# Kernel optimization log

Hardware: AMD Instinct MI355X
Metric: run time of the kernel (lower is better)

## Reference

```python
import jax, jax.numpy as jnp
import numpy as np

N, E = 50000, 800000
IN_DIM, HEADS, OUT_DIM = 128, 4, 32
NEG_SLOPE = 0.2
EPS = 1e-16


def setup_inputs() -> dict:
    key = jax.random.key(0)
    k = jax.random.split(key, 6)
    x = jax.random.normal(k[0], (N, IN_DIM), dtype=jnp.float32)
    edge_index = jax.random.randint(k[1], (2, E), 0, N, dtype=jnp.int64)
    # xavier-uniform-ish params
    lim_w = float(np.sqrt(6.0 / (IN_DIM + HEADS * OUT_DIM)))
    W = jax.random.uniform(k[2], (HEADS * OUT_DIM, IN_DIM), minval=-lim_w, maxval=lim_w, dtype=jnp.float32)
    lim_a = float(np.sqrt(6.0 / (1 + HEADS * OUT_DIM)))
    att_src = jax.random.uniform(k[3], (1, HEADS, OUT_DIM), minval=-lim_a, maxval=lim_a, dtype=jnp.float32)
    att_dst = jax.random.uniform(k[4], (1, HEADS, OUT_DIM), minval=-lim_a, maxval=lim_a, dtype=jnp.float32)
    bias = jnp.zeros((HEADS * OUT_DIM,), dtype=jnp.float32)
    return {"x": x, "edge_index": edge_index, "W": W, "att_src": att_src, "att_dst": att_dst, "bias": bias}


def reference(x, edge_index, W, att_src, att_dst, bias):
    n = x.shape[0]
    h = (x @ W.T).reshape(n, HEADS, OUT_DIM)           # (N,H,D)
    src, dst = edge_index[0], edge_index[1]
    a_src = jnp.sum(h * att_src, axis=-1)              # (N,H)
    a_dst = jnp.sum(h * att_dst, axis=-1)              # (N,H)
    alpha = a_src[src] + a_dst[dst]                    # (E,H)
    alpha = jax.nn.leaky_relu(alpha, NEG_SLOPE)
    # segment (per-dst) softmax over edges, per head
    m = jax.ops.segment_max(alpha, dst, num_segments=n)   # (N,H)
    ex = jnp.exp(alpha - m[dst])
    s = jax.ops.segment_sum(ex, dst, num_segments=n)      # (N,H)
    alpha = ex / (s[dst] + EPS)                            # (E,H)
    # dropout p=0 (eval) -> identity
    msg = h[src] * alpha[..., None]                        # (E,H,D)
    out = jax.ops.segment_sum(msg, dst, num_segments=n)    # (N,H,D)
    out = out.reshape(n, HEADS * OUT_DIM) + bias
    alpha_pooled = alpha.mean(axis=-1)                     # (E,)
    return out, alpha_pooled
```

## Files before the change

### kernel.cpp

```cpp
#include <hip/hip_runtime.h>

#define NNODES 50000
#define NEDGES 800000
#define HD 128
#define NEG 0.2f
#define MTILE 64
#define LDW 136
#define MAXD 64
#define GEMMB ((NNODES + MTILE - 1) / MTILE)
#define NBINS 196
#define CAP 5120
#define GST 16
#define ABLK ((NEDGES + 2047) / 2048)

typedef __attribute__((ext_vector_type(8))) short short8;
typedef __attribute__((ext_vector_type(4))) float floatx4;

static __device__ inline unsigned short f2bf(float f) {
    unsigned u = __float_as_uint(f);
    return (unsigned short)((u + 0x7FFF + ((u >> 16) & 1)) >> 16);
}
static __device__ inline float bf2f(unsigned short u) {
    return __uint_as_float(((unsigned)u) << 16);
}
static __device__ inline float lrelu_exp(float a) {
    a = (a > 0.f) ? a : NEG * a;
    return __expf(a);
}

__global__ __launch_bounds__(256, 4) void gat_main(
    const float* __restrict__ x, const float* __restrict__ W,
    const float* __restrict__ att_src, const float* __restrict__ att_dst,
    const int* __restrict__ ei,
    unsigned short* __restrict__ h, float* __restrict__ asrc,
    float* __restrict__ adst, int* __restrict__ gcnt, int* __restrict__ cbuf)
{
    __shared__ unsigned short Wl[128 * LDW];
    const int t = threadIdx.x;

    if (blockIdx.x >= GEMMB) {
        int* hist = (int*)Wl;
        int* boff = hist + 256;
        const int e0 = (blockIdx.x - GEMMB) * 2048 + t * 8;
        const bool act = (e0 < NEDGES);
        int4 s0 = make_int4(0, 0, 0, 0), s1 = s0, d0 = s0, d1 = s0;
        if (act) {
            s0 = *(const int4*)(ei + e0);
            s1 = *(const int4*)(ei + e0 + 4);
            d0 = *(const int4*)(ei + NEDGES + e0);
            d1 = *(const int4*)(ei + NEDGES + e0 + 4);
        }
        hist[t] = 0;
        __syncthreads();
        if (act) {
            atomicAdd(&hist[d0.x >> 8], 1); atomicAdd(&hist[d0.y >> 8], 1);
            atomicAdd(&hist[d0.z >> 8], 1); atomicAdd(&hist[d0.w >> 8], 1);
            atomicAdd(&hist[d1.x >> 8], 1); atomicAdd(&hist[d1.y >> 8], 1);
            atomicAdd(&hist[d1.z >> 8], 1); atomicAdd(&hist[d1.w >> 8], 1);
        }
        __syncthreads();
        if (t < NBINS && hist[t] > 0)
            boff[t] = atomicAdd(&gcnt[t * GST], hist[t]);
        __syncthreads();
        if (act) {
            int ss[8] = {s0.x, s0.y, s0.z, s0.w, s1.x, s1.y, s1.z, s1.w};
            int dd[8] = {d0.x, d0.y, d0.z, d0.w, d1.x, d1.y, d1.z, d1.w};
#pragma unroll
            for (int j = 0; j < 8; j++) {
                int b = dd[j] >> 8;
                int slot = atomicAdd(&boff[b], 1);
                cbuf[(size_t)b * CAP + slot] = ((dd[j] & 255) << 16) | ss[j];
            }
        }
        return;
    }

    const int rowBase = blockIdx.x * MTILE;

    for (int idx = t * 8; idx < 128 * 128; idx += 2048) {
        int r = idx >> 7, c = idx & 127;
        float4 v0 = *(const float4*)(W + idx);
        float4 v1 = *(const float4*)(W + idx + 4);
        short8 u;
        u[0] = (short)f2bf(v0.x); u[1] = (short)f2bf(v0.y);
        u[2] = (short)f2bf(v0.z); u[3] = (short)f2bf(v0.w);
        u[4] = (short)f2bf(v1.x); u[5] = (short)f2bf(v1.y);
        u[6] = (short)f2bf(v1.z); u[7] = (short)f2bf(v1.w);
        *(short8*)(Wl + r * LDW + c) = u;
    }

    const int wave = t >> 6;
    const int lane = t & 63;
    const int c16  = lane & 15;
    const int quad = lane >> 4;
    const int xr   = rowBase + wave * 16 + c16;
    short8 av[4];
#pragma unroll
    for (int kc = 0; kc < 4; kc++) {
        float4 v0 = make_float4(0.f, 0.f, 0.f, 0.f);
        float4 v1 = v0;
        if (xr < NNODES) {
            const float* p = x + (size_t)xr * 128 + kc * 32 + quad * 8;
            v0 = *(const float4*)p;
            v1 = *(const float4*)(p + 4);
        }
        short8 u;
        u[0] = (short)f2bf(v0.x); u[1] = (short)f2bf(v0.y);
        u[2] = (short)f2bf(v0.z); u[3] = (short)f2bf(v0.w);
        u[4] = (short)f2bf(v1.x); u[5] = (short)f2bf(v1.y);
        u[6] = (short)f2bf(v1.z); u[7] = (short)f2bf(v1.w);
        av[kc] = u;
    }
    __syncthreads();

    floatx4 acc[8];
#pragma unroll
    for (int nt = 0; nt < 8; nt++) acc[nt] = (floatx4)(0.f);

#pragma unroll
    for (int kc = 0; kc < 4; kc++) {
#pragma unroll
        for (int nt = 0; nt < 8; nt++) {
            short8 bv = *(const short8*)(Wl + (nt * 16 + c16) * LDW + kc * 32 + quad * 8);
            acc[nt] = __builtin_amdgcn_mfma_f32_16x16x32_bf16(av[kc], bv, acc[nt], 0, 0, 0);
        }
    }

    float As[8], Ad[8];
#pragma unroll
    for (int nt = 0; nt < 8; nt++) {
        As[nt] = att_src[nt * 16 + c16];
        Ad[nt] = att_dst[nt * 16 + c16];
    }
#pragma unroll
    for (int r = 0; r < 4; r++) {
        const int gr = rowBase + wave * 16 + quad * 4 + r;
#pragma unroll
        for (int hh = 0; hh < 4; hh++) {
            float ps = acc[2 * hh][r] * As[2 * hh] + acc[2 * hh + 1][r] * As[2 * hh + 1];
            float pd = acc[2 * hh][r] * Ad[2 * hh] + acc[2 * hh + 1][r] * Ad[2 * hh + 1];
#pragma unroll
            for (int m = 8; m >= 1; m >>= 1) {
                ps += __shfl_xor(ps, m, 64);
                pd += __shfl_xor(pd, m, 64);
            }
            if (c16 == 0 && gr < NNODES) {
                asrc[gr * 4 + hh] = ps;
                adst[gr * 4 + hh] = pd;
            }
        }
    }

    __syncthreads();
#pragma unroll
    for (int r = 0; r < 4; r++) {
        const int lr = wave * 16 + quad * 4 + r;
#pragma unroll
        for (int nt = 0; nt < 8; nt++)
            Wl[lr * LDW + nt * 16 + c16] = f2bf(acc[nt][r]);
    }
    __syncthreads();
    for (int idx = t * 8; idx < MTILE * 128; idx += 2048) {
        int r = idx >> 7, c = idx & 127;
        int g = rowBase + r;
        if (g < NNODES)
            *(short8*)(h + (size_t)g * HD + c) = *(const short8*)(Wl + r * LDW + c);
    }
}

__global__ __launch_bounds__(1024) void gat_bin(
    const int* __restrict__ gcnt, const int* __restrict__ cbuf,
    int* __restrict__ coff, unsigned short* __restrict__ csr)
{
    __shared__ unsigned short eb[CAP];
    __shared__ int sh[256], hist[256], run[256];
    const int t = threadIdx.x;
    const int b = blockIdx.x;
    const int c_b = gcnt[b * GST];
    const size_t wbase = (size_t)b * CAP;

    if (t < 256) {
        sh[t] = (t < NBINS) ? gcnt[t * GST] : 0;
        hist[t] = 0;
    }
    __syncthreads();
    for (int off = 1; off < 256; off <<= 1) {
        int u = (t < 256 && t >= off) ? sh[t - off] : 0;
        __syncthreads();
        if (t < 256) sh[t] += u;
        __syncthreads();
    }
    const int binbase = sh[b] - c_b;

    for (int i = t; i < c_b; i += 1024)
        atomicAdd(&hist[(cbuf[wbase + i] >> 16) & 255], 1);
    __syncthreads();

    int hv = 0;
    if (t < 256) { hv = hist[t]; sh[t] = hv; }
    __syncthreads();
    for (int off = 1; off < 256; off <<= 1) {
        int u = (t < 256 && t >= off) ? sh[t - off] : 0;
        __syncthreads();
        if (t < 256) sh[t] += u;
        __syncthreads();
    }
    if (t < 256) {
        int ex = sh[t] - hv;
        int n = b * 256 + t;
        if (n < NNODES) coff[n] = binbase + ex;
        run[t] = ex;
    }
    if (b == 0 && t == 0) coff[NNODES] = NEDGES;
    __syncthreads();

    for (int i = t; i < c_b; i += 1024) {
        int e = cbuf[wbase + i];
        int slot = atomicAdd(&run[(e >> 16) & 255], 1);
        eb[slot] = (unsigned short)(e & 0xFFFF);
    }
    __syncthreads();

    for (int i = t; i < c_b; i += 1024)
        csr[binbase + i] = eb[i];
}

__global__ __launch_bounds__(256) void gat_node(
    const int* __restrict__ coff, const unsigned short* __restrict__ csr,
    const float* __restrict__ asrc, const float* __restrict__ adst,
    const unsigned short* __restrict__ h, const float* __restrict__ bias,
    float* __restrict__ out, float* __restrict__ rsumr)
{
    __shared__ unsigned short sh_src[8 * MAXD];
    __shared__ float sh_w[8 * MAXD * 4];
    const int t = threadIdx.x;
    const int node8 = t >> 5;
    const int n = blockIdx.x * 8 + node8;
    const int k = t & 31;
    const int beg = coff[n], end = coff[n + 1];
    const int base = node8 * MAXD;
    const float4 bn = *(const float4*)(adst + n * 4);

    float4 sum = make_float4(0.f, 0.f, 0.f, 0.f);
    for (int j = beg + k; j < end; j += 32) {
        int s = csr[j];
        float4 a = *(const float4*)(asrc + s * 4);
        float4 wv;
        wv.x = lrelu_exp(a.x + bn.x);
        wv.y = lrelu_exp(a.y + bn.y);
        wv.z = lrelu_exp(a.z + bn.z);
        wv.w = lrelu_exp(a.w + bn.w);
        sum.x += wv.x; sum.y += wv.y; sum.z += wv.z; sum.w += wv.w;
        int i = j - beg;
        if (i < MAXD) {
            sh_src[base + i] = (unsigned short)s;
            *(float4*)(sh_w + (base + i) * 4) = wv;
        }
    }
#pragma unroll
    for (int m = 16; m >= 1; m >>= 1) {
        sum.x += __shfl_xor(sum.x, m, 64);
        sum.y += __shfl_xor(sum.y, m, 64);
        sum.z += __shfl_xor(sum.z, m, 64);
        sum.w += __shfl_xor(sum.w, m, 64);
    }
    float rs[4];
    rs[0] = 1.f / (sum.x + 1e-16f);
    rs[1] = 1.f / (sum.y + 1e-16f);
    rs[2] = 1.f / (sum.z + 1e-16f);
    rs[3] = 1.f / (sum.w + 1e-16f);
    if (k == 0)
        *(float4*)(rsumr + n * 4) = make_float4(rs[0], rs[1], rs[2], rs[3]);

    const int half = k >> 4;
    const int i16  = k & 15;
    const int head = i16 >> 2;
    const float rsel = rs[head];
    const int lim = (end - beg < MAXD) ? end - beg : MAXD;

    float accA[8], accB[8];
#pragma unroll
    for (int m = 0; m < 8; m++) { accA[m] = 0.f; accB[m] = 0.f; }

    int j = 0;
    for (; j + 8 <= lim; j += 8) {
        int e0 = j + half, e1 = j + 2 + half, e2 = j + 4 + half, e3 = j + 6 + half;
        int s0 = sh_src[base + e0];
        int s1 = sh_src[base + e1];
        int s2 = sh_src[base + e2];
        int s3 = sh_src[base + e3];
        float w0 = sh_w[(base + e0) * 4 + head] * rsel;
        float w1 = sh_w[(base + e1) * 4 + head] * rsel;
        float w2 = sh_w[(base + e2) * 4 + head] * rsel;
        float w3 = sh_w[(base + e3) * 4 + head] * rsel;
        short8 u0 = *(const short8*)(h + (size_t)s0 * HD + i16 * 8);
        short8 u1 = *(const short8*)(h + (size_t)s1 * HD + i16 * 8);
        short8 u2 = *(const short8*)(h + (size_t)s2 * HD + i16 * 8);
        short8 u3 = *(const short8*)(h + (size_t)s3 * HD + i16 * 8);
#pragma unroll
        for (int m = 0; m < 8; m++) {
            accA[m] = fmaf(bf2f((unsigned short)u0[m]), w0, accA[m]);
            accB[m] = fmaf(bf2f((unsigned short)u1[m]), w1, accB[m]);
            accA[m] = fmaf(bf2f((unsigned short)u2[m]), w2, accA[m]);
            accB[m] = fmaf(bf2f((unsigned short)u3[m]), w3, accB[m]);
        }
    }
    for (; j + 2 <= lim; j += 2) {
        int e0 = j + half;
        int s0 = sh_src[base + e0];
        float w0 = sh_w[(base + e0) * 4 + head] * rsel;
        short8 u0 = *(const short8*)(h + (size_t)s0 * HD + i16 * 8);
#pragma unroll
        for (int m = 0; m < 8; m++)
            accA[m] = fmaf(bf2f((unsigned short)u0[m]), w0, accA[m]);
    }
    if (j < lim && half == 0) {
        int s0 = sh_src[base + j];
        float w0 = sh_w[(base + j) * 4 + head] * rsel;
        short8 u0 = *(const short8*)(h + (size_t)s0 * HD + i16 * 8);
#pragma unroll
        for (int m = 0; m < 8; m++)
            accA[m] = fmaf(bf2f((unsigned short)u0[m]), w0, accA[m]);
    }
    const float bnh = ((const float*)&bn)[head];
    for (int jj = beg + MAXD + half; jj < end; jj += 2) {
        int s0 = csr[jj];
        float w0 = lrelu_exp(asrc[s0 * 4 + head] + bnh) * rsel;
        short8 u0 = *(const short8*)(h + (size_t)s0 * HD + i16 * 8);
#pragma unroll
        for (int m = 0; m < 8; m++)
            accA[m] = fmaf(bf2f((unsigned short)u0[m]), w0, accA[m]);
    }

#pragma unroll
    for (int m = 0; m < 8; m++) {
        accA[m] += accB[m];
        accA[m] += __shfl_xor(accA[m], 16, 64);
    }
    const float4 b4 = *(const float4*)(bias + i16 * 8 + half * 4);
    float4 st;
    st.x = accA[half * 4 + 0] + b4.x;
    st.y = accA[half * 4 + 1] + b4.y;
    st.z = accA[half * 4 + 2] + b4.z;
    st.w = accA[half * 4 + 3] + b4.w;
    *(float4*)(out + (size_t)n * HD + i16 * 8 + half * 4) = st;
}

static __device__ inline float apool1(
    int s, int d, const float* __restrict__ asrc,
    const float* __restrict__ adst, const float* __restrict__ rsumr)
{
    float4 a = *(const float4*)(asrc + s * 4);
    float4 b = *(const float4*)(adst + d * 4);
    float4 r = *(const float4*)(rsumr + d * 4);
    return 0.25f * (lrelu_exp(a.x + b.x) * r.x + lrelu_exp(a.y + b.y) * r.y +
                    lrelu_exp(a.z + b.z) * r.z + lrelu_exp(a.w + b.w) * r.w);
}

__global__ __launch_bounds__(256) void gat_apool(
    const int* __restrict__ ei, const float* __restrict__ asrc,
    const float* __restrict__ adst, const float* __restrict__ rsumr,
    float* __restrict__ apool)
{
    int e0 = (blockIdx.x * 256 + threadIdx.x) * 4;
    if (e0 >= NEDGES) return;
    int4 s = *(const int4*)(ei + e0);
    int4 d = *(const int4*)(ei + NEDGES + e0);
    float4 r;
    r.x = apool1(s.x, d.x, asrc, adst, rsumr);
    r.y = apool1(s.y, d.y, asrc, adst, rsumr);
    r.z = apool1(s.z, d.z, asrc, adst, rsumr);
    r.w = apool1(s.w, d.w, asrc, adst, rsumr);
    *(float4*)(apool + e0) = r;
}

extern "C" void kernel_launch(void* const* d_in, const int* in_sizes, int n_in,
                              void* d_out, int out_size, void* d_ws, size_t ws_size,
                              hipStream_t stream)
{
    const float* x       = (const float*)d_in[0];
    const int*   ei      = (const int*)d_in[1];
    const float* W       = (const float*)d_in[2];
    const float* att_src = (const float*)d_in[3];
    const float* att_dst = (const float*)d_in[4];
    const float* bias    = (const float*)d_in[5];

    float* out   = (float*)d_out;
    float* apool = out + (size_t)NNODES * HD;

    unsigned short* h = (unsigned short*)d_ws;
    float* asrc  = (float*)(h + (size_t)NNODES * HD);
    float* adst  = asrc + NNODES * 4;
    float* rsumr = adst + NNODES * 4;
    int*   gcnt  = (int*)(rsumr + NNODES * 4);
    int*   coff  = gcnt + NBINS * GST;
    int*   cbuf  = coff + NNODES + 4;
    unsigned short* csr = (unsigned short*)(cbuf + (size_t)NBINS * CAP);

    hipMemsetAsync(gcnt, 0, (size_t)NBINS * GST * sizeof(int), stream);

    gat_main<<<GEMMB + ABLK, 256, 0, stream>>>(
        x, W, att_src, att_dst, ei, h, asrc, adst, gcnt, cbuf);
    gat_bin<<<NBINS, 1024, 0, stream>>>(gcnt, cbuf, coff, csr);
    gat_node<<<NNODES / 8, 256, 0, stream>>>(
        coff, csr, asrc, adst, h, bias, out, rsumr);
    gat_apool<<<(NEDGES / 4 + 255) / 256, 256, 0, stream>>>(
        ei, asrc, adst, rsumr, apool);
}
```

Before: 167.7 us.

## Replace global atomic binning with per-block local sort and one wave per node

```diff
diff --git a/kernel.cpp b/kernel.cpp
--- a/kernel.cpp
+++ b/kernel.cpp
@@ -10,7 +10,6 @@
 #define GEMMB ((NNODES + MTILE - 1) / MTILE)
 #define NBINS 196
 #define CAP 5120
-#define GST 16
 #define ABLK ((NEDGES + 2047) / 2048)
 
 typedef __attribute__((ext_vector_type(8))) short short8;
@@ -33,16 +32,20 @@
     const float* __restrict__ att_src, const float* __restrict__ att_dst,
     const int* __restrict__ ei,
     unsigned short* __restrict__ h, float* __restrict__ asrc,
-    float* __restrict__ adst, int* __restrict__ gcnt, int* __restrict__ cbuf)
-{
-    __shared__ unsigned short Wl[128 * LDW];
+    float* __restrict__ adst, int* __restrict__ Sg, int* __restrict__ sbuf)
+{
+    __shared__ __align__(16) unsigned short Wl[128 * LDW];
     const int t = threadIdx.x;
 
     if (blockIdx.x >= GEMMB) {
         int* hist = (int*)Wl;
-        int* boff = hist + 256;
-        const int e0 = (blockIdx.x - GEMMB) * 2048 + t * 8;
+        int* sh   = hist + 256;
+        int* run  = sh + 256;
+        int* lbuf = run + 256;
+        const int blk = blockIdx.x - GEMMB;
+        const int e0 = blk * 2048 + t * 8;
         const bool act = (e0 < NEDGES);
+        const int cnt = (blk == ABLK - 1) ? (NEDGES - blk * 2048) : 2048;
         int4 s0 = make_int4(0, 0, 0, 0), s1 = s0, d0 = s0, d1 = s0;
         if (act) {
             s0 = *(const int4*)(ei + e0);
@@ -59,19 +62,32 @@
             atomicAdd(&hist[d1.z >> 8], 1); atomicAdd(&hist[d1.w >> 8], 1);
         }
         __syncthreads();
-        if (t < NBINS && hist[t] > 0)
-            boff[t] = atomicAdd(&gcnt[t * GST], hist[t]);
+        int hv = hist[t];
+        sh[t] = hv;
+        __syncthreads();
+        for (int off = 1; off < 256; off <<= 1) {
+            int u = (t >= off) ? sh[t - off] : 0;
+            __syncthreads();
+            sh[t] += u;
+            __syncthreads();
+        }
+        int ex = sh[t] - hv;
+        run[t] = ex;
+        Sg[blk * 257 + t] = ex;
+        if (t == 0) Sg[blk * 257 + 256] = cnt;
         __syncthreads();
         if (act) {
             int ss[8] = {s0.x, s0.y, s0.z, s0.w, s1.x, s1.y, s1.z, s1.w};
             int dd[8] = {d0.x, d0.y, d0.z, d0.w, d1.x, d1.y, d1.z, d1.w};
 #pragma unroll
             for (int j = 0; j < 8; j++) {
-                int b = dd[j] >> 8;
-                int slot = atomicAdd(&boff[b], 1);
-                cbuf[(size_t)b * CAP + slot] = ((dd[j] & 255) << 16) | ss[j];
+                int slot = atomicAdd(&run[dd[j] >> 8], 1);
+                lbuf[slot] = ((dd[j] & 255) << 16) | ss[j];
             }
         }
+        __syncthreads();
+        for (int i = t; i < cnt; i += 256)
+            sbuf[blk * 2048 + i] = lbuf[i];
         return;
     }
 
@@ -169,20 +185,51 @@
 }
 
 __global__ __launch_bounds__(1024) void gat_bin(
-    const int* __restrict__ gcnt, const int* __restrict__ cbuf,
-    int* __restrict__ coff, unsigned short* __restrict__ csr)
-{
-    __shared__ unsigned short eb[CAP];
-    __shared__ int sh[256], hist[256], run[256];
+    const int* __restrict__ Sg, const int* __restrict__ sbuf,
+    int* __restrict__ coffB, int* __restrict__ coffE,
+    unsigned short* __restrict__ csr)
+{
+    __shared__ int s0arr[391];
+    __shared__ int segoff[391];
+    __shared__ int ebi[CAP];
+    __shared__ unsigned short ebs[CAP];
+    __shared__ int hist[256], run[256], sh[512];
     const int t = threadIdx.x;
     const int b = blockIdx.x;
-    const int c_b = gcnt[b * GST];
-    const size_t wbase = (size_t)b * CAP;
-
-    if (t < 256) {
-        sh[t] = (t < NBINS) ? gcnt[t * GST] : 0;
-        hist[t] = 0;
-    }
+
+    int s0v = 0, lenv = 0;
+    if (t < 391) {
+        s0v = Sg[t * 257 + b];
+        lenv = Sg[t * 257 + b + 1] - s0v;
+        s0arr[t] = s0v;
+    }
+    if (t < 256) hist[t] = 0;
+    if (t < 512) sh[t] = (t < 391) ? lenv : 0;
+    __syncthreads();
+    for (int off = 1; off < 512; off <<= 1) {
+        int u = (t < 512 && t >= off) ? sh[t - off] : 0;
+        __syncthreads();
+        if (t < 512) sh[t] += u;
+        __syncthreads();
+    }
+    if (t < 391) segoff[t] = sh[t] - lenv;
+    __syncthreads();
+    const int c_b = sh[390];
+
+    for (int i = t; i < c_b; i += 1024) {
+        int lo = 0, hi = 390;
+        while (lo < hi) {
+            int mid = (lo + hi + 1) >> 1;
+            if (segoff[mid] <= i) lo = mid; else hi = mid - 1;
+        }
+        int e = sbuf[lo * 2048 + s0arr[lo] + (i - segoff[lo])];
+        ebi[i] = e;
+        atomicAdd(&hist[(e >> 16) & 255], 1);
+    }
+    __syncthreads();
+
+    int hv = (t < 256) ? hist[t] : 0;
+    if (t < 256) sh[t] = hv;
     __syncthreads();
     for (int off = 1; off < 256; off <<= 1) {
         int u = (t < 256 && t >= off) ? sh[t - off] : 0;
@@ -190,59 +237,47 @@
         if (t < 256) sh[t] += u;
         __syncthreads();
     }
-    const int binbase = sh[b] - c_b;
-
-    for (int i = t; i < c_b; i += 1024)
-        atomicAdd(&hist[(cbuf[wbase + i] >> 16) & 255], 1);
-    __syncthreads();
-
-    int hv = 0;
-    if (t < 256) { hv = hist[t]; sh[t] = hv; }
-    __syncthreads();
-    for (int off = 1; off < 256; off <<= 1) {
-        int u = (t < 256 && t >= off) ? sh[t - off] : 0;
-        __syncthreads();
-        if (t < 256) sh[t] += u;
-        __syncthreads();
-    }
     if (t < 256) {
         int ex = sh[t] - hv;
+        run[t] = ex;
         int n = b * 256 + t;
-        if (n < NNODES) coff[n] = binbase + ex;
-        run[t] = ex;
-    }
-    if (b == 0 && t == 0) coff[NNODES] = NEDGES;
+        if (n < NNODES) {
+            coffB[n] = b * CAP + ex;
+            coffE[n] = b * CAP + ex + hv;
+        }
+    }
     __syncthreads();
 
     for (int i = t; i < c_b; i += 1024) {
-        int e = cbuf[wbase + i];
+        int e = ebi[i];
         int slot = atomicAdd(&run[(e >> 16) & 255], 1);
-        eb[slot] = (unsigned short)(e & 0xFFFF);
+        ebs[slot] = (unsigned short)(e & 0xFFFF);
     }
     __syncthreads();
 
     for (int i = t; i < c_b; i += 1024)
-        csr[binbase + i] = eb[i];
+        csr[(size_t)b * CAP + i] = ebs[i];
 }
 
 __global__ __launch_bounds__(256) void gat_node(
-    const int* __restrict__ coff, const unsigned short* __restrict__ csr,
+    const int* __restrict__ coffB, const int* __restrict__ coffE,
+    const unsigned short* __restrict__ csr,
     const float* __restrict__ asrc, const float* __restrict__ adst,
     const unsigned short* __restrict__ h, const float* __restrict__ bias,
     float* __restrict__ out, float* __restrict__ rsumr)
 {
-    __shared__ unsigned short sh_src[8 * MAXD];
-    __shared__ float sh_w[8 * MAXD * 4];
+    __shared__ unsigned short sh_src[4 * MAXD];
+    __shared__ float sh_w[4 * MAXD * 4];
     const int t = threadIdx.x;
-    const int node8 = t >> 5;
-    const int n = blockIdx.x * 8 + node8;
-    const int k = t & 31;
-    const int beg = coff[n], end = coff[n + 1];
-    const int base = node8 * MAXD;
+    const int w = t >> 6;
+    const int lane = t & 63;
+    const int n = blockIdx.x * 4 + w;
+    const int beg = coffB[n], end = coffE[n];
+    const int base = w * MAXD;
     const float4 bn = *(const float4*)(adst + n * 4);
 
     float4 sum = make_float4(0.f, 0.f, 0.f, 0.f);
-    for (int j = beg + k; j < end; j += 32) {
+    for (int j = beg + lane; j < end; j += 64) {
         int s = csr[j];
         float4 a = *(const float4*)(asrc + s * 4);
         float4 wv;
@@ -258,7 +293,7 @@
         }
     }
 #pragma unroll
-    for (int m = 16; m >= 1; m >>= 1) {
+    for (int m = 32; m >= 1; m >>= 1) {
         sum.x += __shfl_xor(sum.x, m, 64);
         sum.y += __shfl_xor(sum.y, m, 64);
         sum.z += __shfl_xor(sum.z, m, 64);
@@ -269,11 +304,11 @@
     rs[1] = 1.f / (sum.y + 1e-16f);
     rs[2] = 1.f / (sum.z + 1e-16f);
     rs[3] = 1.f / (sum.w + 1e-16f);
-    if (k == 0)
+    if (lane == 0)
         *(float4*)(rsumr + n * 4) = make_float4(rs[0], rs[1], rs[2], rs[3]);
 
-    const int half = k >> 4;
-    const int i16  = k & 15;
+    const int quad = lane >> 4;
+    const int i16  = lane & 15;
     const int head = i16 >> 2;
     const float rsel = rs[head];
     const int lim = (end - beg < MAXD) ? end - beg : MAXD;
@@ -283,8 +318,8 @@
     for (int m = 0; m < 8; m++) { accA[m] = 0.f; accB[m] = 0.f; }
 
     int j = 0;
-    for (; j + 8 <= lim; j += 8) {
-        int e0 = j + half, e1 = j + 2 + half, e2 = j + 4 + half, e3 = j + 6 + half;
+    for (; j + 16 <= lim; j += 16) {
+        int e0 = j + quad, e1 = j + 4 + quad, e2 = j + 8 + quad, e3 = j + 12 + quad;
         int s0 = sh_src[base + e0];
         int s1 = sh_src[base + e1];
         int s2 = sh_src[base + e2];
@@ -305,8 +340,8 @@
             accB[m] = fmaf(bf2f((unsigned short)u3[m]), w3, accB[m]);
         }
     }
-    for (; j + 2 <= lim; j += 2) {
-        int e0 = j + half;
+    for (; j + 4 <= lim; j += 4) {
+        int e0 = j + quad;
         int s0 = sh_src[base + e0];
         float w0 = sh_w[(base + e0) * 4 + head] * rsel;
         short8 u0 = *(const short8*)(h + (size_t)s0 * HD + i16 * 8);
@@ -314,16 +349,17 @@
         for (int m = 0; m < 8; m++)
             accA[m] = fmaf(bf2f((unsigned short)u0[m]), w0, accA[m]);
     }
-    if (j < lim && half == 0) {
-        int s0 = sh_src[base + j];
-        float w0 = sh_w[(base + j) * 4 + head] * rsel;
+    if (quad < lim - j) {
+        int s0 = sh_src[base + j + quad];
+        float w0 = sh_w[(base + j + quad) * 4 + head] * rsel;
         short8 u0 = *(const short8*)(h + (size_t)s0 * HD + i16 * 8);
 #pragma unroll
         for (int m = 0; m < 8; m++)
             accA[m] = fmaf(bf2f((unsigned short)u0[m]), w0, accA[m]);
     }
-    const float bnh = ((const float*)&bn)[head];
-    for (int jj = beg + MAXD + half; jj < end; jj += 2) {
+    const float bnh = (head == 0) ? bn.x : (head == 1) ? bn.y
+                     : (head == 2) ? bn.z : bn.w;
+    for (int jj = beg + MAXD + quad; jj < end; jj += 4) {
         int s0 = csr[jj];
         float w0 = lrelu_exp(asrc[s0 * 4 + head] + bnh) * rsel;
         short8 u0 = *(const short8*)(h + (size_t)s0 * HD + i16 * 8);
@@ -336,14 +372,20 @@
     for (int m = 0; m < 8; m++) {
         accA[m] += accB[m];
         accA[m] += __shfl_xor(accA[m], 16, 64);
-    }
-    const float4 b4 = *(const float4*)(bias + i16 * 8 + half * 4);
-    float4 st;
-    st.x = accA[half * 4 + 0] + b4.x;
-    st.y = accA[half * 4 + 1] + b4.y;
-    st.z = accA[half * 4 + 2] + b4.z;
-    st.w = accA[half * 4 + 3] + b4.w;
-    *(float4*)(out + (size_t)n * HD + i16 * 8 + half * 4) = st;
+        accA[m] += __shfl_xor(accA[m], 32, 64);
+    }
+    if (quad < 2) {
+        const float4 b4 = *(const float4*)(bias + i16 * 8 + quad * 4);
+        float4 st;
+        if (quad == 0) {
+            st.x = accA[0] + b4.x; st.y = accA[1] + b4.y;
+            st.z = accA[2] + b4.z; st.w = accA[3] + b4.w;
+        } else {
+            st.x = accA[4] + b4.x; st.y = accA[5] + b4.y;
+            st.z = accA[6] + b4.z; st.w = accA[7] + b4.w;
+        }
+        *(float4*)(out + (size_t)n * HD + i16 * 8 + quad * 4) = st;
+    }
 }
 
 static __device__ inline float apool1(
@@ -392,18 +434,17 @@
     float* asrc  = (float*)(h + (size_t)NNODES * HD);
     float* adst  = asrc + NNODES * 4;
     float* rsumr = adst + NNODES * 4;
-    int*   gcnt  = (int*)(rsumr + NNODES * 4);
-    int*   coff  = gcnt + NBINS * GST;
-    int*   cbuf  = coff + NNODES + 4;
-    unsigned short* csr = (unsigned short*)(cbuf + (size_t)NBINS * CAP);
-
-    hipMemsetAsync(gcnt, 0, (size_t)NBINS * GST * sizeof(int), stream);
+    int*   Sg    = (int*)(rsumr + NNODES * 4);
+    int*   coffB = Sg + ABLK * 257 + 4;
+    int*   coffE = coffB + NNODES + 4;
+    int*   sbuf  = coffE + NNODES + 4;
+    unsigned short* csr = (unsigned short*)(sbuf + (size_t)ABLK * 2048);
 
     gat_main<<<GEMMB + ABLK, 256, 0, stream>>>(
-        x, W, att_src, att_dst, ei, h, asrc, adst, gcnt, cbuf);
-    gat_bin<<<NBINS, 1024, 0, stream>>>(gcnt, cbuf, coff, csr);
-    gat_node<<<NNODES / 8, 256, 0, stream>>>(
-        coff, csr, asrc, adst, h, bias, out, rsumr);
+        x, W, att_src, att_dst, ei, h, asrc, adst, Sg, sbuf);
+    gat_bin<<<NBINS, 1024, 0, stream>>>(Sg, sbuf, coffB, coffE, csr);
+    gat_node<<<NNODES / 4, 256, 0, stream>>>(
+        coffB, coffE, csr, asrc, adst, h, bias, out, rsumr);
     gat_apool<<<(NEDGES / 4 + 255) / 256, 256, 0, stream>>>(
         ei, asrc, adst, rsumr, apool);
 }
```

New measurement: 160.1 us. -4.6%, faster.
